# Kernel optimization log

Measured on AMD Instinct MI355X. Metric: run time of the kernel, lower is better.

Reference implementation:

```python
import jax, jax.numpy as jnp
import numpy as np

PROCESS_INIT = 1.0
OBSERVATION_INIT = 1.0


def _build_dynamics_A(K, fut_len):
    # shift-structured single-modal A: state slot i takes value of slot i+1, last step repeats
    sd = 2 * fut_len
    a = np.zeros((sd, sd), dtype=np.float32)
    for i in range(fut_len - 1):
        a[2 * i, 2 * i + 2] = 1.0
        a[2 * i + 1, 2 * i + 3] = 1.0
    a[sd - 2, sd - 2] = 1.0
    a[sd - 1, sd - 1] = 1.0
    # block-diagonal over K modes
    return jnp.asarray(np.kron(np.eye(K, dtype=np.float32), a))


def setup_inputs() -> dict:
    key = jax.random.key(0)
    ks = jax.random.split(key, 6)
    B, A, K, fut_len = 2, 32, 6, 30
    D = K * 2 * fut_len  # 360
    belief_mean = jax.random.normal(ks[0], (B, A, D), dtype=jnp.float32)
    M = jax.random.normal(ks[1], (B, A, D, D), dtype=jnp.float32)
    # symmetric, SPD (eigenvalues ~ 2 +/- 0.2) so linear solves are well-posed
    belief_covariance = 0.003 * (M + jnp.swapaxes(M, -1, -2)) + 2.0 * jnp.eye(D, dtype=jnp.float32)
    observations = jax.random.normal(ks[2], (B, A, D), dtype=jnp.float32)
    rs = jax.random.uniform(ks[3], (B, A), dtype=jnp.float32)
    initialized = jax.random.bernoulli(ks[4], 0.7, (B, A))
    selected = jax.random.bernoulli(ks[5], 0.8, (B, A))
    return {
        "belief_mean": belief_mean,
        "belief_covariance": belief_covariance,
        "observations": observations,
        "rs": rs,
        "initialized": initialized,
        "selected": selected,
        "K": K,
        "fut_len": fut_len,
    }


def reference(belief_mean, belief_covariance, observations, rs, initialized, selected, K, fut_len):
    D = K * 2 * fut_len
    A = _build_dynamics_A(K, fut_len)  # [D, D], static sparse shift structure
    I = jnp.eye(D, dtype=belief_mean.dtype)
    r_obs = (rs + OBSERVATION_INIT)[..., None, None]  # [B, A, 1, 1]

    init_new = selected & (~initialized)  # first observation of agent
    upd = selected & initialized          # predict + Kalman update

    # --- initialization branch ---
    mean_init = observations
    cov_init = belief_covariance + r_obs * I

    # --- predict step: m <- A m ; P <- A P A^T + Q, Q = process_init * I ---
    m_pred = belief_mean @ A.T  # [B, A, D]
    P_pred = jnp.einsum('ij,bnjk,lk->bnil', A, belief_covariance, A) + PROCESS_INIT * I

    # --- update step (H = I): S = P + R ; Kg = P S^{-1} ---
    S = P_pred + r_obs * I
    Kg = P_pred @ jnp.linalg.inv(S)
    m_upd = m_pred + jnp.einsum('bnij,bnj->bni', Kg, observations - m_pred)
    P_upd = (I - Kg) @ P_pred

    # --- scatter the three branches back (masked merge) ---
    mean_out = jnp.where(init_new[..., None], mean_init,
               jnp.where(upd[..., None], m_upd, belief_mean))
    cov_out = jnp.where(init_new[..., None, None], cov_init,
              jnp.where(upd[..., None, None], P_upd, belief_covariance))
    initialized_out = initialized | selected
    return mean_out, cov_out, initialized_out
```

## Files before the change

kernel.cpp:

```cpp
#include <hip/hip_runtime.h>

#define D 360
#define NAG 64
#define NB 120
#define NPAN 3
#define COV_OFF (NAG * D)
#define INIT_OFF (COV_OFF + NAG * D * D)
#define SB(par, ag, slot) ((((size_t)(par) * NAG + (ag)) * 4 + (slot)) * 7200)

__device__ __forceinline__ int gshift(int i) {
    return ((i % 60) < 58) ? (i + 2) : i;
}

__global__ __launch_bounds__(384) void build_kernel(
    const float* __restrict__ P, const float* __restrict__ mean_in,
    const float* __restrict__ obs, const float* __restrict__ rs,
    const int* __restrict__ init_f, const int* __restrict__ sel_f,
    float* __restrict__ out, float* __restrict__ rb)
{
    const int by = blockIdx.x, ag = blockIdx.y, t = threadIdx.x;
    const bool ini = init_f[ag] != 0, sel = sel_f[ag] != 0;
    const float c = rs[ag] + 1.0f;
    if (by == 45) {
        if (t < D) {
            float v = (sel && !ini) ? obs[ag * D + t] : mean_in[ag * D + t];
            out[ag * D + t] = v;
        }
        if (t == 0) out[INIT_OFF + ag] = (ini || sel) ? 1.0f : 0.0f;
        return;
    }
    if (t >= D) return;
    const float* Pa = P + (size_t)ag * D * D;
    float* cov = out + COV_OFF + (size_t)ag * D * D;
    const int j = t;
    if (sel && ini) {
        const int gj = gshift(j);
        #pragma unroll
        for (int s = 0; s < 8; ++s) {
            const int i = by * 8 + s;
            float v = Pa[(size_t)gshift(i) * D + gj];
            if (i == j) v += 1.0f + c;
            cov[(size_t)i * D + j] = v;
            if (i < NB && j >= NB)
                rb[SB(0, ag, j / 60 - 2) + i * 60 + (j % 60)] = v;
        }
    } else if (sel) {
        #pragma unroll
        for (int s = 0; s < 8; ++s) {
            const int i = by * 8 + s;
            cov[(size_t)i * D + j] = Pa[(size_t)i * D + j] + ((i == j) ? c : 0.0f);
        }
    } else {
        #pragma unroll
        for (int s = 0; s < 8; ++s) {
            const int i = by * 8 + s;
            cov[(size_t)i * D + j] = Pa[(size_t)i * D + j];
        }
    }
}

__device__ __forceinline__ void inv4(float4& m0, float4& m1, float4& m2, float4& m3)
{
    float pv, f;
    pv = 1.0f / m0.x;
    m0.y *= pv; m0.z *= pv; m0.w *= pv; m0.x = pv;
    f = m1.x; m1.y = fmaf(-f, m0.y, m1.y); m1.z = fmaf(-f, m0.z, m1.z); m1.w = fmaf(-f, m0.w, m1.w); m1.x = -f * pv;
    f = m2.x; m2.y = fmaf(-f, m0.y, m2.y); m2.z = fmaf(-f, m0.z, m2.z); m2.w = fmaf(-f, m0.w, m2.w); m2.x = -f * pv;
    f = m3.x; m3.y = fmaf(-f, m0.y, m3.y); m3.z = fmaf(-f, m0.z, m3.z); m3.w = fmaf(-f, m0.w, m3.w); m3.x = -f * pv;
    pv = 1.0f / m1.y;
    m1.x *= pv; m1.z *= pv; m1.w *= pv; m1.y = pv;
    f = m0.y; m0.x = fmaf(-f, m1.x, m0.x); m0.z = fmaf(-f, m1.z, m0.z); m0.w = fmaf(-f, m1.w, m0.w); m0.y = -f * pv;
    f = m2.y; m2.x = fmaf(-f, m1.x, m2.x); m2.z = fmaf(-f, m1.z, m2.z); m2.w = fmaf(-f, m1.w, m2.w); m2.y = -f * pv;
    f = m3.y; m3.x = fmaf(-f, m1.x, m3.x); m3.z = fmaf(-f, m1.z, m3.z); m3.w = fmaf(-f, m1.w, m3.w); m3.y = -f * pv;
    pv = 1.0f / m2.z;
    m2.x *= pv; m2.y *= pv; m2.w *= pv; m2.z = pv;
    f = m0.z; m0.x = fmaf(-f, m2.x, m0.x); m0.y = fmaf(-f, m2.y, m0.y); m0.w = fmaf(-f, m2.w, m0.w); m0.z = -f * pv;
    f = m1.z; m1.x = fmaf(-f, m2.x, m1.x); m1.y = fmaf(-f, m2.y, m1.y); m1.w = fmaf(-f, m2.w, m1.w); m1.z = -f * pv;
    f = m3.z; m3.x = fmaf(-f, m2.x, m3.x); m3.y = fmaf(-f, m2.y, m3.y); m3.w = fmaf(-f, m2.w, m3.w); m3.z = -f * pv;
    pv = 1.0f / m3.w;
    m3.x *= pv; m3.y *= pv; m3.z *= pv; m3.w = pv;
    f = m0.w; m0.x = fmaf(-f, m3.x, m0.x); m0.y = fmaf(-f, m3.y, m0.y); m0.z = fmaf(-f, m3.z, m0.z); m0.w = -f * pv;
    f = m1.w; m1.x = fmaf(-f, m3.x, m1.x); m1.y = fmaf(-f, m3.y, m1.y); m1.z = fmaf(-f, m3.z, m1.z); m1.w = -f * pv;
    f = m2.w; m2.x = fmaf(-f, m3.x, m2.x); m2.y = fmaf(-f, m3.y, m2.y); m2.z = fmaf(-f, m3.z, m2.z); m2.w = -f * pv;
}

#define NQ 30
struct Slab {
    float4 v0, v1, v2, v3, v4, v5, v6, v7, v8, v9,
           v10, v11, v12, v13, v14, v15, v16, v17, v18, v19,
           v20, v21, v22, v23, v24, v25, v26, v27, v28, v29;
};
template<int I> __device__ __forceinline__ float4& AT(Slab& s) {
    if constexpr (I == 0) return s.v0;   else if constexpr (I == 1) return s.v1;
    else if constexpr (I == 2) return s.v2;  else if constexpr (I == 3) return s.v3;
    else if constexpr (I == 4) return s.v4;  else if constexpr (I == 5) return s.v5;
    else if constexpr (I == 6) return s.v6;  else if constexpr (I == 7) return s.v7;
    else if constexpr (I == 8) return s.v8;  else if constexpr (I == 9) return s.v9;
    else if constexpr (I == 10) return s.v10; else if constexpr (I == 11) return s.v11;
    else if constexpr (I == 12) return s.v12; else if constexpr (I == 13) return s.v13;
    else if constexpr (I == 14) return s.v14; else if constexpr (I == 15) return s.v15;
    else if constexpr (I == 16) return s.v16; else if constexpr (I == 17) return s.v17;
    else if constexpr (I == 18) return s.v18; else if constexpr (I == 19) return s.v19;
    else if constexpr (I == 20) return s.v20; else if constexpr (I == 21) return s.v21;
    else if constexpr (I == 22) return s.v22; else if constexpr (I == 23) return s.v23;
    else if constexpr (I == 24) return s.v24; else if constexpr (I == 25) return s.v25;
    else if constexpr (I == 26) return s.v26; else if constexpr (I == 27) return s.v27;
    else if constexpr (I == 28) return s.v28; else return s.v29;
}
template<int Q = 0> __device__ __forceinline__ void slab_load(Slab& s, const float* src) {
    if constexpr (Q < NQ) { AT<Q>(s) = *(const float4*)(src + 4 * Q); slab_load<Q + 1>(s, src); }
}
template<int Q = 0> __device__ __forceinline__ void slab_store(Slab& s, float* dst) {
    if constexpr (Q < NQ) { *(float4*)(dst + 4 * Q) = AT<Q>(s); slab_store<Q + 1>(s, dst); }
}
template<int Q = 0> __device__ __forceinline__ void slab_stage(Slab& s, float4 (&dst)[NQ]) {
    if constexpr (Q < NQ) { dst[Q] = AT<Q>(s); slab_stage<Q + 1>(s, dst); }
}
template<int Q = 0> __device__ __forceinline__ void slab_store_stash(
    Slab& s, float* rb_base, size_t stride_slot, int nrel) {
    if constexpr (Q < NQ) {
        float* dst = rb_base + (Q >= 15 ? stride_slot : 0) + nrel * 60 + (Q % 15) * 4;
        *(float4*)dst = AT<Q>(s);
        slab_store_stash<Q + 1>(s, rb_base, stride_slot, nrel);
    }
}
template<int KB, int Q = 0> __device__ __forceinline__ void zero_except(Slab& s) {
    if constexpr (Q < NQ) {
        if constexpr (Q != KB) AT<Q>(s) = make_float4(0.f, 0.f, 0.f, 0.f);
        zero_except<KB, Q + 1>(s);
    }
}
template<int KB, int Q = 0>
__device__ __forceinline__ void rank4(Slab& s, const float4 sc, const float4 (&pb)[4][NQ]) {
    if constexpr (Q < NQ) {
        if constexpr (Q != KB) {
            const float4 p0 = pb[0][Q], p1 = pb[1][Q], p2 = pb[2][Q], p3 = pb[3][Q];
            float4& r = AT<Q>(s);
            r.x = fmaf(sc.x, p0.x, fmaf(sc.y, p1.x, fmaf(sc.z, p2.x, fmaf(sc.w, p3.x, r.x))));
            r.y = fmaf(sc.x, p0.y, fmaf(sc.y, p1.y, fmaf(sc.z, p2.y, fmaf(sc.w, p3.y, r.y))));
            r.z = fmaf(sc.x, p0.z, fmaf(sc.y, p1.z, fmaf(sc.z, p2.z, fmaf(sc.w, p3.z, r.z))));
            r.w = fmaf(sc.x, p0.w, fmaf(sc.y, p1.w, fmaf(sc.z, p2.w, fmaf(sc.w, p3.w, r.w))));
        }
        rank4<KB, Q + 1>(s, sc, pb);
    }
}
template<int Q = 0>
__device__ __forceinline__ void slab_store_fin(Slab& s, float* dst, int r, int j0,
                                               float c, float c2) {
    if constexpr (Q < NQ) {
        const int cg = j0 + 4 * Q;
        const float4 v = AT<Q>(s);
        float4 o;
        o.x = ((r == cg + 0) ? c : 0.f) - c2 * v.x;
        o.y = ((r == cg + 1) ? c : 0.f) - c2 * v.y;
        o.z = ((r == cg + 2) ? c : 0.f) - c2 * v.z;
        o.w = ((r == cg + 3) ? c : 0.f) - c2 * v.w;
        *(float4*)(dst + 4 * Q) = o;
        slab_store_fin<Q + 1>(s, dst, r, j0, c, c2);
    }
}

template<int KB>
__device__ __forceinline__ void gj_step(Slab& s, int r, int rel, float4 (&praw)[2][4][NQ])
{
    const int buf = KB & 1;
    float4 m0 = praw[buf][0][KB];
    float4 m1 = praw[buf][1][KB];
    float4 m2 = praw[buf][2][KB];
    float4 m3 = praw[buf][3][KB];
    inv4(m0, m1, m2, m3);
    if (r < D) {
        const bool is_piv = (rel >= 4 * KB) && (rel < 4 * KB + 4);
        float4 sc;
        if (is_piv) {
            const int i = rel - 4 * KB;
            sc = (i == 0) ? m0 : (i == 1) ? m1 : (i == 2) ? m2 : m3;
            zero_except<KB>(s);
        } else {
            const float4 fr = AT<KB>(s);
            sc.x = -(fr.x * m0.x + fr.y * m1.x + fr.z * m2.x + fr.w * m3.x);
            sc.y = -(fr.x * m0.y + fr.y * m1.y + fr.z * m2.y + fr.w * m3.y);
            sc.z = -(fr.x * m0.z + fr.y * m1.z + fr.z * m2.z + fr.w * m3.z);
            sc.w = -(fr.x * m0.w + fr.y * m1.w + fr.z * m2.w + fr.w * m3.w);
        }
        rank4<KB>(s, sc, praw[buf]);
        AT<KB>(s) = sc;
        if (KB < NQ - 1 && rel >= 4 * (KB + 1) && rel < 4 * (KB + 1) + 4) {
            slab_stage(s, praw[buf ^ 1][rel - 4 * (KB + 1)]);
        }
    }
    __syncthreads();
}

template<int KB> struct GJ {
    __device__ static __forceinline__ void run(Slab& s, int r, int rel,
                                               float4 (&praw)[2][4][NQ]) {
        gj_step<KB>(s, r, rel, praw);
        GJ<KB + 1>::run(s, r, rel, praw);
    }
};
template<> struct GJ<NQ> {
    __device__ static __forceinline__ void run(Slab&, int, int, float4 (&)[2][4][NQ]) {}
};

__global__ __launch_bounds__(384, 1) void factor_kernel(
    float* __restrict__ out, const float* __restrict__ rs,
    const int* __restrict__ init_f, const int* __restrict__ sel_f,
    float* __restrict__ rb, int p)
{
    const int ag = blockIdx.x;
    if (!(init_f[ag] && sel_f[ag])) return;
    float* M = out + COV_OFF + (size_t)ag * D * D;
    const int j0 = p * NB;
    const int r = threadIdx.x;
    const int rel = r - j0;
    Slab s;
    if (r < D) slab_load(s, M + (size_t)r * D + j0);
    __shared__ float4 praw[2][4][NQ];
    if (rel >= 0 && rel < 4) slab_stage(s, praw[0][rel]);
    __syncthreads();
    GJ<0>::run(s, r, rel, praw);
    if (r < D) {
        float* dst = M + (size_t)r * D + j0;
        if (p == NPAN - 1) {
            const float c = rs[ag] + 1.0f;
            slab_store_fin(s, dst, r, j0, c, c * c);
        } else {
            slab_store(s, dst);
            const int nrel = r - NB * (p + 1);
            if (nrel >= 0 && nrel < NB) {
                float* rb_base = rb + SB((p + 1) & 1, ag, 2 * p);
                slab_store_stash(s, rb_base, (size_t)7200, nrel);
            }
        }
    }
}

__device__ __forceinline__ void mm_row(const float4 a, const float4 b0, const float4 b1,
                                       const float4 b2, const float4 b3, float acc[4]) {
    acc[0] = fmaf(a.x, b0.x, fmaf(a.y, b1.x, fmaf(a.z, b2.x, fmaf(a.w, b3.x, acc[0]))));
    acc[1] = fmaf(a.x, b0.y, fmaf(a.y, b1.y, fmaf(a.z, b2.y, fmaf(a.w, b3.y, acc[1]))));
    acc[2] = fmaf(a.x, b0.z, fmaf(a.y, b1.z, fmaf(a.z, b2.z, fmaf(a.w, b3.z, acc[2]))));
    acc[3] = fmaf(a.x, b0.w, fmaf(a.y, b1.w, fmaf(a.z, b2.w, fmaf(a.w, b3.w, acc[3]))));
}

__global__ __launch_bounds__(256) void update_kernel(
    float* __restrict__ out, const float* __restrict__ rs,
    const int* __restrict__ init_f, const int* __restrict__ sel_f,
    float* __restrict__ rb, int p)
{
    const int ag = blockIdx.x;
    if (!(init_f[ag] && sel_f[ag])) return;
    const int y = blockIdx.y;
    const int ct = y + (y >= 2 * p ? 2 : 0);
    const int rt = blockIdx.z;
    const int r0 = 60 * rt, c0 = 60 * ct;
    const bool panelrow = ((rt >> 1) == p);
    float* M = out + COV_OFF + (size_t)ag * D * D;
    const float c = rs[ag] + 1.0f;
    const float c2 = c * c;
    __shared__ float R[NB][60];
    __shared__ float F[60][NB + 4];
    const int t = threadIdx.x;
    {
        const float* rsrc = rb + SB(p & 1, ag, y);
        for (int idx = t; idx < 120 * 15; idx += 256) {
            const int k = idx / 15, q = idx % 15;
            *(float4*)&R[k][4 * q] = *(const float4*)(rsrc + k * 60 + 4 * q);
        }
    }
    {
        for (int idx = t; idx < 60 * NQ; idx += 256) {
            const int row = idx / NQ, q = idx % NQ;
            float4 v = *(const float4*)(M + (size_t)(r0 + row) * D + p * NB + 4 * q);
            if (p == NPAN - 1) {
                const int rg = r0 + row, cg = p * NB + 4 * q;
                v.x = (((rg == cg + 0) ? c : 0.f) - v.x) / c2;
                v.y = (((rg == cg + 1) ? c : 0.f) - v.y) / c2;
                v.z = (((rg == cg + 2) ? c : 0.f) - v.z) / c2;
                v.w = (((rg == cg + 3) ? c : 0.f) - v.w) / c2;
            }
            *(float4*)&F[row][4 * q] = v;
        }
    }
    __syncthreads();
    const int tx = t % 16, ty = t / 16;
    if (tx < 15 && ty < 15) {
        float acc[4][4];
        #pragma unroll
        for (int i = 0; i < 4; ++i)
            #pragma unroll
            for (int j = 0; j < 4; ++j) acc[i][j] = 0.0f;
        for (int kq = 0; kq < NQ; ++kq) {
            float4 a0 = *(const float4*)&F[4 * ty + 0][4 * kq];
            float4 a1 = *(const float4*)&F[4 * ty + 1][4 * kq];
            float4 a2 = *(const float4*)&F[4 * ty + 2][4 * kq];
            float4 a3 = *(const float4*)&F[4 * ty + 3][4 * kq];
            float4 b0 = *(const float4*)&R[4 * kq + 0][4 * tx];
            float4 b1 = *(const float4*)&R[4 * kq + 1][4 * tx];
            float4 b2 = *(const float4*)&R[4 * kq + 2][4 * tx];
            float4 b3 = *(const float4*)&R[4 * kq + 3][4 * tx];
            mm_row(a0, b0, b1, b2, b3, acc[0]);
            mm_row(a1, b0, b1, b2, b3, acc[1]);
            mm_row(a2, b0, b1, b2, b3, acc[2]);
            mm_row(a3, b0, b1, b2, b3, acc[3]);
        }
        #pragma unroll
        for (int i = 0; i < 4; ++i) {
            const int rg = r0 + 4 * ty + i;
            float* dst = M + (size_t)rg * D + c0 + 4 * tx;
            float4 base;
            if (panelrow) { base = make_float4(0.f, 0.f, 0.f, 0.f); }
            else          { base = *(const float4*)dst; }
            float4 v;
            v.x = base.x + acc[i][0];
            v.y = base.y + acc[i][1];
            v.z = base.z + acc[i][2];
            v.w = base.w + acc[i][3];
            if (p < NPAN - 1) {
                if ((rt >> 1) == p + 1 && (ct >> 1) != p + 1) {
                    const int slot = ct - (ct > 2 * p + 3 ? 2 : 0);
                    const int srow = rg - NB * (p + 1);
                    *(float4*)(rb + SB((p + 1) & 1, ag, slot) + srow * 60 + 4 * tx) = v;
                }
                *(float4*)dst = v;
            } else {
                const int cg = c0 + 4 * tx;
                float4 o;
                o.x = ((rg == cg + 0) ? c : 0.f) - c2 * v.x;
                o.y = ((rg == cg + 1) ? c : 0.f) - c2 * v.y;
                o.z = ((rg == cg + 2) ? c : 0.f) - c2 * v.z;
                o.w = ((rg == cg + 3) ? c : 0.f) - c2 * v.w;
                *(float4*)dst = o;
            }
        }
    }
}

__global__ __launch_bounds__(384) void solve_mean_kernel(
    float* __restrict__ out, const float* __restrict__ mean_in,
    const float* __restrict__ obs, const float* __restrict__ rs,
    const int* __restrict__ init_f, const int* __restrict__ sel_f)
{
    const int ag = blockIdx.x;
    if (!(init_f[ag] && sel_f[ag])) return;
    const float* C = out + COV_OFF + (size_t)ag * D * D;
    __shared__ float dsh[D];
    const int t = threadIdx.x;
    if (t < D) dsh[t] = obs[ag * D + t] - mean_in[ag * D + gshift(t)];
    __syncthreads();
    if (t < D) {
        float dot = 0.0f;
        #pragma unroll 8
        for (int j = 0; j < D; ++j)
            dot = fmaf(C[(size_t)j * D + t], dsh[j], dot);
        const float c = rs[ag] + 1.0f;
        out[ag * D + t] = obs[ag * D + t] - dsh[t] + dot / c;
    }
}

extern "C" void kernel_launch(void* const* d_in, const int* in_sizes, int n_in,
                              void* d_out, int out_size, void* d_ws, size_t ws_size,
                              hipStream_t stream) {
    const float* mean_in     = (const float*)d_in[0];
    const float* P           = (const float*)d_in[1];
    const float* obs         = (const float*)d_in[2];
    const float* rs          = (const float*)d_in[3];
    const int*   initialized = (const int*)d_in[4];
    const int*   selected    = (const int*)d_in[5];
    float* out = (float*)d_out;
    float* rb  = (float*)d_ws;

    build_kernel<<<dim3(46, NAG), 384, 0, stream>>>(P, mean_in, obs, rs,
                                                    initialized, selected, out, rb);
    for (int p = 0; p < NPAN; ++p) {
        factor_kernel<<<NAG, 384, 0, stream>>>(out, rs, initialized, selected, rb, p);
        update_kernel<<<dim3(NAG, 4, 6), 256, 0, stream>>>(out, rs, initialized,
                                                           selected, rb, p);
    }
    solve_mean_kernel<<<NAG, 384, 0, stream>>>(out, mean_in, obs, rs, initialized, selected);
}
```

Measured before the change: 364.6 us.

## Split Gauss-Jordan panel rows across two half-threads in factor kernel

```diff
diff --git a/kernel.cpp b/kernel.cpp
--- a/kernel.cpp
+++ b/kernel.cpp
@@ -4,6 +4,7 @@
 #define NAG 64
 #define NB 120
 #define NPAN 3
+#define NQG 30
 #define COV_OFF (NAG * D)
 #define INIT_OFF (COV_OFF + NAG * D * D)
 #define SB(par, ag, slot) ((((size_t)(par) * NAG + (ag)) * 4 + (slot)) * 7200)
@@ -84,11 +85,8 @@
     f = m2.w; m2.x = fmaf(-f, m3.x, m2.x); m2.y = fmaf(-f, m3.y, m2.y); m2.z = fmaf(-f, m3.z, m2.z); m2.w = -f * pv;
 }
 
-#define NQ 30
 struct Slab {
-    float4 v0, v1, v2, v3, v4, v5, v6, v7, v8, v9,
-           v10, v11, v12, v13, v14, v15, v16, v17, v18, v19,
-           v20, v21, v22, v23, v24, v25, v26, v27, v28, v29;
+    float4 v0, v1, v2, v3, v4, v5, v6, v7, v8, v9, v10, v11, v12, v13, v14;
 };
 template<int I> __device__ __forceinline__ float4& AT(Slab& s) {
     if constexpr (I == 0) return s.v0;   else if constexpr (I == 1) return s.v1;
@@ -98,57 +96,40 @@
     else if constexpr (I == 8) return s.v8;  else if constexpr (I == 9) return s.v9;
     else if constexpr (I == 10) return s.v10; else if constexpr (I == 11) return s.v11;
     else if constexpr (I == 12) return s.v12; else if constexpr (I == 13) return s.v13;
-    else if constexpr (I == 14) return s.v14; else if constexpr (I == 15) return s.v15;
-    else if constexpr (I == 16) return s.v16; else if constexpr (I == 17) return s.v17;
-    else if constexpr (I == 18) return s.v18; else if constexpr (I == 19) return s.v19;
-    else if constexpr (I == 20) return s.v20; else if constexpr (I == 21) return s.v21;
-    else if constexpr (I == 22) return s.v22; else if constexpr (I == 23) return s.v23;
-    else if constexpr (I == 24) return s.v24; else if constexpr (I == 25) return s.v25;
-    else if constexpr (I == 26) return s.v26; else if constexpr (I == 27) return s.v27;
-    else if constexpr (I == 28) return s.v28; else return s.v29;
+    else return s.v14;
 }
 template<int Q = 0> __device__ __forceinline__ void slab_load(Slab& s, const float* src) {
-    if constexpr (Q < NQ) { AT<Q>(s) = *(const float4*)(src + 4 * Q); slab_load<Q + 1>(s, src); }
+    if constexpr (Q < 15) { AT<Q>(s) = *(const float4*)(src + 4 * Q); slab_load<Q + 1>(s, src); }
 }
 template<int Q = 0> __device__ __forceinline__ void slab_store(Slab& s, float* dst) {
-    if constexpr (Q < NQ) { *(float4*)(dst + 4 * Q) = AT<Q>(s); slab_store<Q + 1>(s, dst); }
-}
-template<int Q = 0> __device__ __forceinline__ void slab_stage(Slab& s, float4 (&dst)[NQ]) {
-    if constexpr (Q < NQ) { dst[Q] = AT<Q>(s); slab_stage<Q + 1>(s, dst); }
-}
-template<int Q = 0> __device__ __forceinline__ void slab_store_stash(
-    Slab& s, float* rb_base, size_t stride_slot, int nrel) {
-    if constexpr (Q < NQ) {
-        float* dst = rb_base + (Q >= 15 ? stride_slot : 0) + nrel * 60 + (Q % 15) * 4;
-        *(float4*)dst = AT<Q>(s);
-        slab_store_stash<Q + 1>(s, rb_base, stride_slot, nrel);
-    }
-}
-template<int KB, int Q = 0> __device__ __forceinline__ void zero_except(Slab& s) {
-    if constexpr (Q < NQ) {
-        if constexpr (Q != KB) AT<Q>(s) = make_float4(0.f, 0.f, 0.f, 0.f);
-        zero_except<KB, Q + 1>(s);
-    }
-}
-template<int KB, int Q = 0>
-__device__ __forceinline__ void rank4(Slab& s, const float4 sc, const float4 (&pb)[4][NQ]) {
-    if constexpr (Q < NQ) {
-        if constexpr (Q != KB) {
-            const float4 p0 = pb[0][Q], p1 = pb[1][Q], p2 = pb[2][Q], p3 = pb[3][Q];
+    if constexpr (Q < 15) { *(float4*)(dst + 4 * Q) = AT<Q>(s); slab_store<Q + 1>(s, dst); }
+}
+template<int Q = 0> __device__ __forceinline__ void stage_row(Slab& s, float4* rowp) {
+    if constexpr (Q < 15) { rowp[Q] = AT<Q>(s); stage_row<Q + 1>(s, rowp); }
+}
+template<int Q = 0> __device__ __forceinline__ void zero_all(Slab& s) {
+    if constexpr (Q < 15) { AT<Q>(s) = make_float4(0.f, 0.f, 0.f, 0.f); zero_all<Q + 1>(s); }
+}
+template<int OFF, int SKIP, int Q = 0>
+__device__ __forceinline__ void rank4g(Slab& s, const float4 sc, const float4 (&pb)[4][NQG]) {
+    if constexpr (Q < 15) {
+        if constexpr (Q != SKIP) {
+            const float4 p0 = pb[0][OFF + Q], p1 = pb[1][OFF + Q],
+                         p2 = pb[2][OFF + Q], p3 = pb[3][OFF + Q];
             float4& r = AT<Q>(s);
             r.x = fmaf(sc.x, p0.x, fmaf(sc.y, p1.x, fmaf(sc.z, p2.x, fmaf(sc.w, p3.x, r.x))));
             r.y = fmaf(sc.x, p0.y, fmaf(sc.y, p1.y, fmaf(sc.z, p2.y, fmaf(sc.w, p3.y, r.y))));
             r.z = fmaf(sc.x, p0.z, fmaf(sc.y, p1.z, fmaf(sc.z, p2.z, fmaf(sc.w, p3.z, r.z))));
             r.w = fmaf(sc.x, p0.w, fmaf(sc.y, p1.w, fmaf(sc.z, p2.w, fmaf(sc.w, p3.w, r.w))));
         }
-        rank4<KB, Q + 1>(s, sc, pb);
+        rank4g<OFF, SKIP, Q + 1>(s, sc, pb);
     }
 }
 template<int Q = 0>
-__device__ __forceinline__ void slab_store_fin(Slab& s, float* dst, int r, int j0,
+__device__ __forceinline__ void slab_store_fin(Slab& s, float* dst, int r, int j0h,
                                                float c, float c2) {
-    if constexpr (Q < NQ) {
-        const int cg = j0 + 4 * Q;
+    if constexpr (Q < 15) {
+        const int cg = j0h + 4 * Q;
         const float4 v = AT<Q>(s);
         float4 o;
         o.x = ((r == cg + 0) ? c : 0.f) - c2 * v.x;
@@ -156,54 +137,66 @@
         o.z = ((r == cg + 2) ? c : 0.f) - c2 * v.z;
         o.w = ((r == cg + 3) ? c : 0.f) - c2 * v.w;
         *(float4*)(dst + 4 * Q) = o;
-        slab_store_fin<Q + 1>(s, dst, r, j0, c, c2);
+        slab_store_fin<Q + 1>(s, dst, r, j0h, c, c2);
     }
 }
 
 template<int KB>
-__device__ __forceinline__ void gj_step(Slab& s, int r, int rel, float4 (&praw)[2][4][NQ])
-{
-    const int buf = KB & 1;
-    float4 m0 = praw[buf][0][KB];
-    float4 m1 = praw[buf][1][KB];
-    float4 m2 = praw[buf][2][KB];
-    float4 m3 = praw[buf][3][KB];
+__device__ __forceinline__ void gj_step(Slab& s, int r, int rel, int h,
+                                        float4 (&praw)[2][4][NQG],
+                                        float4 (&fcol)[2][D])
+{
+    constexpr int BUF = KB & 1;
+    constexpr int H = KB / 15;
+    constexpr int Q = KB % 15;
+    float4 m0 = praw[BUF][0][KB], m1 = praw[BUF][1][KB],
+           m2 = praw[BUF][2][KB], m3 = praw[BUF][3][KB];
     inv4(m0, m1, m2, m3);
     if (r < D) {
-        const bool is_piv = (rel >= 4 * KB) && (rel < 4 * KB + 4);
+        const bool ispiv = (rel >= 4 * KB) && (rel < 4 * KB + 4);
         float4 sc;
-        if (is_piv) {
+        if (ispiv) {
             const int i = rel - 4 * KB;
             sc = (i == 0) ? m0 : (i == 1) ? m1 : (i == 2) ? m2 : m3;
-            zero_except<KB>(s);
+            zero_all(s);
         } else {
-            const float4 fr = AT<KB>(s);
+            const float4 fr = fcol[BUF][r];
             sc.x = -(fr.x * m0.x + fr.y * m1.x + fr.z * m2.x + fr.w * m3.x);
             sc.y = -(fr.x * m0.y + fr.y * m1.y + fr.z * m2.y + fr.w * m3.y);
             sc.z = -(fr.x * m0.z + fr.y * m1.z + fr.z * m2.z + fr.w * m3.z);
             sc.w = -(fr.x * m0.w + fr.y * m1.w + fr.z * m2.w + fr.w * m3.w);
         }
-        rank4<KB>(s, sc, praw[buf]);
-        AT<KB>(s) = sc;
-        if (KB < NQ - 1 && rel >= 4 * (KB + 1) && rel < 4 * (KB + 1) + 4) {
-            slab_stage(s, praw[buf ^ 1][rel - 4 * (KB + 1)]);
+        if (h == H) {
+            rank4g<H * 15, Q>(s, sc, praw[BUF]);
+            AT<Q>(s) = sc;
+        } else {
+            rank4g<(1 - H) * 15, -1>(s, sc, praw[BUF]);
+        }
+        if constexpr (KB < NQG - 1) {
+            constexpr int H2 = (KB + 1) / 15;
+            constexpr int Q2 = (KB + 1) % 15;
+            if (h == H2) fcol[BUF ^ 1][r] = AT<Q2>(s);
+            const int nrel = rel - 4 * (KB + 1);
+            if (nrel >= 0 && nrel < 4) stage_row(s, &praw[BUF ^ 1][nrel][h * 15]);
         }
     }
     __syncthreads();
 }
 
 template<int KB> struct GJ {
-    __device__ static __forceinline__ void run(Slab& s, int r, int rel,
-                                               float4 (&praw)[2][4][NQ]) {
-        gj_step<KB>(s, r, rel, praw);
-        GJ<KB + 1>::run(s, r, rel, praw);
+    static __device__ __forceinline__ void run(Slab& s, int r, int rel, int h,
+                                               float4 (&praw)[2][4][NQG],
+                                               float4 (&fcol)[2][D]) {
+        gj_step<KB>(s, r, rel, h, praw, fcol);
+        GJ<KB + 1>::run(s, r, rel, h, praw, fcol);
     }
 };
-template<> struct GJ<NQ> {
-    __device__ static __forceinline__ void run(Slab&, int, int, float4 (&)[2][4][NQ]) {}
+template<> struct GJ<NQG> {
+    static __device__ __forceinline__ void run(Slab&, int, int, int,
+                                               float4 (&)[2][4][NQG], float4 (&)[2][D]) {}
 };
 
-__global__ __launch_bounds__(384, 1) void factor_kernel(
+__global__ __launch_bounds__(768, 3) void factor_kernel(
     float* __restrict__ out, const float* __restrict__ rs,
     const int* __restrict__ init_f, const int* __restrict__ sel_f,
     float* __restrict__ rb, int p)
@@ -212,26 +205,32 @@
     if (!(init_f[ag] && sel_f[ag])) return;
     float* M = out + COV_OFF + (size_t)ag * D * D;
     const int j0 = p * NB;
-    const int r = threadIdx.x;
+    const int t = threadIdx.x;
+    const int h = (t >= 384) ? 1 : 0;
+    const int r = t - 384 * h;
     const int rel = r - j0;
+    __shared__ float4 praw[2][4][NQG];
+    __shared__ float4 fcol[2][D];
     Slab s;
-    if (r < D) slab_load(s, M + (size_t)r * D + j0);
-    __shared__ float4 praw[2][4][NQ];
-    if (rel >= 0 && rel < 4) slab_stage(s, praw[0][rel]);
+    if (r < D) {
+        slab_load(s, M + (size_t)r * D + j0 + h * 60);
+        if (rel >= 0 && rel < 4) stage_row(s, &praw[0][rel][h * 15]);
+        if (h == 0) fcol[0][r] = s.v0;
+    }
     __syncthreads();
-    GJ<0>::run(s, r, rel, praw);
+    GJ<0>::run(s, r, rel, h, praw, fcol);
+    const float c = rs[ag] + 1.0f;
+    const float c2 = c * c;
     if (r < D) {
-        float* dst = M + (size_t)r * D + j0;
+        const int j0h = j0 + h * 60;
+        float* dst = M + (size_t)r * D + j0h;
         if (p == NPAN - 1) {
-            const float c = rs[ag] + 1.0f;
-            slab_store_fin(s, dst, r, j0, c, c * c);
+            slab_store_fin(s, dst, r, j0h, c, c2);
         } else {
             slab_store(s, dst);
             const int nrel = r - NB * (p + 1);
-            if (nrel >= 0 && nrel < NB) {
-                float* rb_base = rb + SB((p + 1) & 1, ag, 2 * p);
-                slab_store_stash(s, rb_base, (size_t)7200, nrel);
-            }
+            if (nrel >= 0 && nrel < NB)
+                slab_store(s, rb + SB((p + 1) & 1, ag, 2 * p + h) + nrel * 60);
         }
     }
 }
@@ -270,8 +269,8 @@
         }
     }
     {
-        for (int idx = t; idx < 60 * NQ; idx += 256) {
-            const int row = idx / NQ, q = idx % NQ;
+        for (int idx = t; idx < 60 * NQG; idx += 256) {
+            const int row = idx / NQG, q = idx % NQG;
             float4 v = *(const float4*)(M + (size_t)(r0 + row) * D + p * NB + 4 * q);
             if (p == NPAN - 1) {
                 const int rg = r0 + row, cg = p * NB + 4 * q;
@@ -291,7 +290,7 @@
         for (int i = 0; i < 4; ++i)
             #pragma unroll
             for (int j = 0; j < 4; ++j) acc[i][j] = 0.0f;
-        for (int kq = 0; kq < NQ; ++kq) {
+        for (int kq = 0; kq < NQG; ++kq) {
             float4 a0 = *(const float4*)&F[4 * ty + 0][4 * kq];
             float4 a1 = *(const float4*)&F[4 * ty + 1][4 * kq];
             float4 a2 = *(const float4*)&F[4 * ty + 2][4 * kq];
@@ -374,7 +373,7 @@
     build_kernel<<<dim3(46, NAG), 384, 0, stream>>>(P, mean_in, obs, rs,
                                                     initialized, selected, out, rb);
     for (int p = 0; p < NPAN; ++p) {
-        factor_kernel<<<NAG, 384, 0, stream>>>(out, rs, initialized, selected, rb, p);
+        factor_kernel<<<NAG, 768, 0, stream>>>(out, rs, initialized, selected, rb, p);
         update_kernel<<<dim3(NAG, 4, 6), 256, 0, stream>>>(out, rs, initialized,
                                                            selected, rb, p);
     }
```

Result: slower. 381.3 us (+4.6%).
